# Kernel tuning notes

Measured on AMD Instinct MI355X. Metric: run time of the kernel, lower is better.

The kernel has to match this reference:

```python
import jax, jax.numpy as jnp
import numpy as np

HSP, WSP = 8, 32
HEADS = 6
EPS = 1e-5


def _ln(x, g, b):
    m = x.mean(-1, keepdims=True)
    v = ((x - m) ** 2).mean(-1, keepdims=True)
    return (x - m) / jnp.sqrt(v + EPS) * g + b


def _pos_mlp(rpe, pw0, pb0, g1, be1, w1, b1, g2, be2, w2, b2, g3, be3, w3, b3):
    # DynamicPosBias (residual=False): pos3(pos2(pos1(pos_proj(biases))))
    x = rpe @ pw0.T + pb0
    x = jax.nn.relu(_ln(x, g1, be1)) @ w1.T + b1
    x = jax.nn.relu(_ln(x, g2, be2)) @ w2.T + b2
    x = jax.nn.relu(_ln(x, g3, be3)) @ w3.T + b3
    return x  # (n_bias, HEADS)


def setup_inputs() -> dict:
    key = jax.random.key(0)
    ks = jax.random.split(key, 8)
    B, H, W, C = 4, 128, 256, 192
    L = H * W
    pd = (C // 4) // 4  # pos_dim = 12
    nbias = (2 * HSP - 1) * (2 * WSP - 1)  # 945
    N = HSP * WSP  # 256
    nW = L // N  # 128
    f32 = jnp.float32
    return {
        "qkv": jax.random.normal(ks[0], (3, B, L, C), f32),
        "mask": jax.random.normal(ks[1], (nW, N, N), f32),
        "rpe_biases": jax.random.normal(ks[2], (nbias, 2), f32),
        "pw0": jax.random.normal(ks[3], (pd, 2), f32) * 0.02,
        "pb0": jnp.zeros((pd,), f32),
        "g1": jnp.ones((pd,), f32),
        "be1": jnp.zeros((pd,), f32),
        "w1": jax.random.normal(ks[4], (pd, pd), f32) * 0.02,
        "b1": jnp.zeros((pd,), f32),
        "g2": jnp.ones((pd,), f32),
        "be2": jnp.zeros((pd,), f32),
        "w2": jax.random.normal(ks[5], (pd, pd), f32) * 0.02,
        "b2": jnp.zeros((pd,), f32),
        "g3": jnp.ones((pd,), f32),
        "be3": jnp.zeros((pd,), f32),
        "w3": jax.random.normal(ks[6], (HEADS, pd), f32) * 0.02,
        "b3": jnp.zeros((HEADS,), f32),
        "rpi": jax.random.randint(ks[7], (N, N), 0, nbias),
        "H": H,
        "W": W,
    }


def reference(qkv, mask, rpe_biases, pw0, pb0, g1, be1, w1, b1, g2, be2, w2, b2, g3, be3, w3, b3, rpi, H, W):
    _, B, L, C = qkv.shape
    hd = C // HEADS
    scale = hd ** -0.5
    N = HSP * WSP

    def im2win(x):  # (B,L,C) -> (B*nW, HEADS, N, hd)
        x = x.reshape(B, H // HSP, HSP, W // WSP, WSP, C)
        x = x.transpose(0, 1, 3, 2, 4, 5).reshape(-1, N, HEADS, hd)
        return x.transpose(0, 2, 1, 3)

    q = im2win(qkv[0]) * scale
    k = im2win(qkv[1])
    v = im2win(qkv[2])
    attn = jnp.einsum('whnd,whmd->whnm', q, k)  # (B*nW, HEADS, N, N)
    pos = _pos_mlp(rpe_biases, pw0, pb0, g1, be1, w1, b1, g2, be2, w2, b2, g3, be3, w3, b3)
    rpb = pos[rpi.reshape(-1)].reshape(N, N, HEADS).transpose(2, 0, 1)  # (HEADS,N,N)
    attn = attn + rpb[None]
    nW = mask.shape[0]
    attn = attn.reshape(B, nW, HEADS, N, N) + mask[None, :, None]
    attn = jax.nn.softmax(attn, axis=-1).reshape(-1, HEADS, N, N)
    x = (attn @ v).transpose(0, 2, 1, 3).reshape(-1, N, C)  # (B*nW, N, C)
    # windows2img
    x = x.reshape(B, H // HSP, W // WSP, HSP, WSP, C).transpose(0, 1, 3, 2, 4, 5).reshape(B, H, W, C)
    return x
```

## Files before the change

### kernel.cpp

```cpp
#include <hip/hip_runtime.h>

#define EPS 1e-5f
#define SCALE 0.17677669529663687f

typedef __attribute__((ext_vector_type(8))) short bf16x8;
typedef __attribute__((ext_vector_type(4))) float f32x4;

__device__ __forceinline__ unsigned short f2bf(float f) {
  unsigned u = __float_as_uint(f);
  return (unsigned short)((u + 0x7FFFu + ((u >> 16) & 1u)) >> 16);
}
__device__ __forceinline__ float bf2f(unsigned short h) {
  return __uint_as_float(((unsigned)h) << 16);
}
__device__ __forceinline__ float bflo(unsigned u) { return __uint_as_float(u << 16); }
__device__ __forceinline__ float bfhi(unsigned u) { return __uint_as_float(u & 0xFFFF0000u); }

__device__ __forceinline__ int bias_sidx(int row, int col) {
  return ((row >> 2) << 10) + ((col >> 5) << 7) + ((col & 15) << 3) + (((col >> 4) & 1) << 2) + (row & 3);
}

__global__ void pos_mlp_kernel(const float* __restrict__ rpe,
                               const float* __restrict__ pw0, const float* __restrict__ pb0,
                               const float* __restrict__ g1, const float* __restrict__ be1,
                               const float* __restrict__ w1, const float* __restrict__ b1,
                               const float* __restrict__ g2, const float* __restrict__ be2,
                               const float* __restrict__ w2, const float* __restrict__ b2,
                               const float* __restrict__ g3, const float* __restrict__ be3,
                               const float* __restrict__ w3, const float* __restrict__ b3,
                               float* __restrict__ posT) {
  int r = blockIdx.x * blockDim.x + threadIdx.x;
  if (r >= 945) return;
  float a = rpe[2 * r], c = rpe[2 * r + 1];
  float x[12], y[12];
#pragma unroll
  for (int i = 0; i < 12; ++i) x[i] = pw0[2 * i] * a + pw0[2 * i + 1] * c + pb0[i];

  auto stage = [&](const float* g, const float* be, const float* w, const float* bb,
                   const float* in, float* outv, int dout) {
    float m = 0.f;
#pragma unroll
    for (int i = 0; i < 12; ++i) m += in[i];
    m *= (1.f / 12.f);
    float v = 0.f;
#pragma unroll
    for (int i = 0; i < 12; ++i) { float d = in[i] - m; v += d * d; }
    v *= (1.f / 12.f);
    float rs = rsqrtf(v + EPS);
    float t[12];
#pragma unroll
    for (int i = 0; i < 12; ++i) t[i] = fmaxf((in[i] - m) * rs * g[i] + be[i], 0.f);
    for (int o = 0; o < dout; ++o) {
      float s = bb[o];
#pragma unroll
      for (int i = 0; i < 12; ++i) s += w[o * 12 + i] * t[i];
      outv[o] = s;
    }
  };
  stage(g1, be1, w1, b1, x, y, 12);
  stage(g2, be2, w2, b2, y, x, 12);
  stage(g3, be3, w3, b3, x, y, 6);
#pragma unroll
  for (int h = 0; h < 6; ++h) posT[h * 945 + r] = y[h];
}

__global__ void rpb_gather_swz(const int* __restrict__ rpi, const float* __restrict__ posT,
                               unsigned short* __restrict__ rpb) {
  int n2 = blockIdx.x * 256 + threadIdx.x;
  int row = n2 >> 8, col = n2 & 255;
  int idx = rpi[n2];
  int s = bias_sidx(row, col);
#pragma unroll
  for (int h = 0; h < 6; ++h) rpb[(h << 16) + s] = f2bf(posT[h * 945 + idx]);
}

__global__ void mask_cvt_swz(const float* __restrict__ src, uint4* __restrict__ dst) {
  int g = blockIdx.x * 256 + threadIdx.x;
  int wimg = g >> 13;
  int rem = g & 8191;
  int rg = rem >> 7;
  int cc = (rem >> 4) & 7;
  int l16 = rem & 15;
  const float* m = src + (wimg << 16);
  unsigned v[8];
#pragma unroll
  for (int ct = 0; ct < 2; ++ct)
#pragma unroll
    for (int r = 0; r < 4; ++r)
      v[ct * 4 + r] = f2bf(m[(rg * 4 + r) * 256 + cc * 32 + ct * 16 + l16]);
  uint4 o;
  o.x = v[0] | (v[1] << 16);
  o.y = v[2] | (v[3] << 16);
  o.z = v[4] | (v[5] << 16);
  o.w = v[6] | (v[7] << 16);
  dst[(wimg << 13) + (rg << 7) + (cc << 4) + l16] = o;
}

template <int USEBF>
__global__ __launch_bounds__(512, 4) void attn_kernel(
    const float* __restrict__ qkv, const float* __restrict__ maskf,
    const unsigned short* __restrict__ maskb, const unsigned short* __restrict__ rpb,
    float* __restrict__ out) {
  __shared__ unsigned short Kb[10240];
  __shared__ unsigned short Vt[8448];
  __shared__ unsigned short Pl[10240];

  const int tid = threadIdx.x;
  const int wv = tid >> 6;
  const int lane = tid & 63;
  const int quad = lane >> 4;
  const int l16 = lane & 15;
  const int wIdx = blockIdx.x, h = blockIdx.y;
  const int b = wIdx >> 7, wimg = wIdx & 127;
  const int wh = wimg >> 3, ww = wimg & 7;

  {
    const int tok = tid >> 3;
    const int c4 = (tid & 7) << 2;
#pragma unroll
    for (int p = 0; p < 4; ++p) {
      int n = (p << 6) + tok;
      int i = n >> 5, j = n & 31;
      int l = ((wh << 3) + i) * 256 + (ww << 5) + j;
      const float* kp = qkv + ((size_t)((4 + b) * 32768 + l)) * 192 + h * 32 + c4;
      const float* vp = qkv + ((size_t)((8 + b) * 32768 + l)) * 192 + h * 32 + c4;
      float4 kk = *(const float4*)kp;
      float4 vvv = *(const float4*)vp;
      unsigned long long pk = (unsigned long long)f2bf(kk.x) |
                              ((unsigned long long)f2bf(kk.y) << 16) |
                              ((unsigned long long)f2bf(kk.z) << 32) |
                              ((unsigned long long)f2bf(kk.w) << 48);
      *(unsigned long long*)(&Kb[n * 40 + c4]) = pk;
      int tokp = (n & ~31) | (((n & 15) << 1) + ((n >> 4) & 1));
      Vt[(c4 + 0) * 264 + tokp] = f2bf(vvv.x);
      Vt[(c4 + 1) * 264 + tokp] = f2bf(vvv.y);
      Vt[(c4 + 2) * 264 + tokp] = f2bf(vvv.z);
      Vt[(c4 + 3) * 264 + tokp] = f2bf(vvv.w);
    }
  }

  bf16x8 qf[2];
#pragma unroll
  for (int rt = 0; rt < 2; ++rt) {
    int n = (wv << 5) + (rt << 4) + l16;
    int i = n >> 5, j = n & 31;
    int l = ((wh << 3) + i) * 256 + (ww << 5) + j;
    const float* qp = qkv + ((size_t)(b * 32768 + l)) * 192 + h * 32 + (quad << 3);
    float4 a0 = *(const float4*)qp;
    float4 a1 = *(const float4*)(qp + 4);
    bf16x8 f;
    f[0] = (short)f2bf(a0.x * SCALE); f[1] = (short)f2bf(a0.y * SCALE);
    f[2] = (short)f2bf(a0.z * SCALE); f[3] = (short)f2bf(a0.w * SCALE);
    f[4] = (short)f2bf(a1.x * SCALE); f[5] = (short)f2bf(a1.y * SCALE);
    f[6] = (short)f2bf(a1.z * SCALE); f[7] = (short)f2bf(a1.w * SCALE);
    qf[rt] = f;
  }

  __syncthreads();

  f32x4 Oacc[2][2];
#pragma unroll
  for (int rt = 0; rt < 2; ++rt) {
    Oacc[rt][0] = (f32x4){0.f, 0.f, 0.f, 0.f};
    Oacc[rt][1] = (f32x4){0.f, 0.f, 0.f, 0.f};
  }
  float lsum[2][4] = {};

  const uint4* mb4 = (const uint4*)maskb + ((size_t)wimg << 13);
  const uint4* rb4 = (const uint4*)rpb + ((size_t)h << 13);
  const float* mfp0 = maskf + ((size_t)wimg << 16);
  unsigned short* Plw = &Pl[wv * 1280];
  const f32x4 zero = (f32x4){0.f, 0.f, 0.f, 0.f};

  for (int cc = 0; cc < 8; ++cc) {
    const int cb = cc << 5;
    uint4 mu[2], ru[2];
#pragma unroll
    for (int rt = 0; rt < 2; ++rt) {
      int rg = (wv << 3) + (rt << 2) + quad;
      int bidx = (rg << 7) + (cc << 4) + l16;
      ru[rt] = rb4[bidx];
      if (USEBF) mu[rt] = mb4[bidx];
    }
    bf16x8 kf0 = *(const bf16x8*)(&Kb[(cb + l16) * 40 + (quad << 3)]);
    bf16x8 kf1 = *(const bf16x8*)(&Kb[(cb + 16 + l16) * 40 + (quad << 3)]);
    f32x4 S[2][2];
#pragma unroll
    for (int rt = 0; rt < 2; ++rt) {
      S[rt][0] = __builtin_amdgcn_mfma_f32_16x16x32_bf16(qf[rt], kf0, zero, 0, 0, 0);
      S[rt][1] = __builtin_amdgcn_mfma_f32_16x16x32_bf16(qf[rt], kf1, zero, 0, 0, 0);
    }
#pragma unroll
    for (int rt = 0; rt < 2; ++rt) {
      float m0[4], m1[4], p0[4], p1[4];
      if (USEBF) {
        m0[0] = bflo(mu[rt].x); m0[1] = bfhi(mu[rt].x); m0[2] = bflo(mu[rt].y); m0[3] = bfhi(mu[rt].y);
        m1[0] = bflo(mu[rt].z); m1[1] = bfhi(mu[rt].z); m1[2] = bflo(mu[rt].w); m1[3] = bfhi(mu[rt].w);
      } else {
        int row0 = (wv << 5) + (rt << 4) + (quad << 2);
#pragma unroll
        for (int r = 0; r < 4; ++r) {
          m0[r] = mfp0[(row0 + r) * 256 + cb + l16];
          m1[r] = mfp0[(row0 + r) * 256 + cb + 16 + l16];
        }
      }
      p0[0] = bflo(ru[rt].x); p0[1] = bfhi(ru[rt].x); p0[2] = bflo(ru[rt].y); p0[3] = bfhi(ru[rt].y);
      p1[0] = bflo(ru[rt].z); p1[1] = bfhi(ru[rt].z); p1[2] = bflo(ru[rt].w); p1[3] = bfhi(ru[rt].w);
#pragma unroll
      for (int r = 0; r < 4; ++r) {
        float e0 = __expf(S[rt][0][r] + m0[r] + p0[r]);
        float e1 = __expf(S[rt][1][r] + m1[r] + p1[r]);
        lsum[rt][r] += e0 + e1;
        unsigned pw = (unsigned)f2bf(e0) | ((unsigned)f2bf(e1) << 16);
        *(unsigned*)(&Plw[((rt << 4) + (quad << 2) + r) * 40 + (l16 << 1)]) = pw;
      }
    }
    bf16x8 pf[2];
#pragma unroll
    for (int rt = 0; rt < 2; ++rt)
      pf[rt] = *(const bf16x8*)(&Plw[((rt << 4) + l16) * 40 + (quad << 3)]);
    bf16x8 vf0 = *(const bf16x8*)(&Vt[l16 * 264 + cb + (quad << 3)]);
    bf16x8 vf1 = *(const bf16x8*)(&Vt[(16 + l16) * 264 + cb + (quad << 3)]);
#pragma unroll
    for (int rt = 0; rt < 2; ++rt) {
      Oacc[rt][0] = __builtin_amdgcn_mfma_f32_16x16x32_bf16(pf[rt], vf0, Oacc[rt][0], 0, 0, 0);
      Oacc[rt][1] = __builtin_amdgcn_mfma_f32_16x16x32_bf16(pf[rt], vf1, Oacc[rt][1], 0, 0, 0);
    }
  }

#pragma unroll
  for (int rt = 0; rt < 2; ++rt) {
    int n0 = (wv << 5) + (rt << 4) + (quad << 2);
#pragma unroll
    for (int r = 0; r < 4; ++r) {
      float v = lsum[rt][r];
      v += __shfl_xor(v, 1);
      v += __shfl_xor(v, 2);
      v += __shfl_xor(v, 4);
      v += __shfl_xor(v, 8);
      float inv = 1.0f / v;
      int n = n0 + r;
      int i = n >> 5, j = n & 31;
      size_t o = ((size_t)((b * 128 + (wh << 3) + i) * 256 + (ww << 5) + j)) * 192 + h * 32 + l16;
      out[o] = Oacc[rt][0][r] * inv;
      out[o + 16] = Oacc[rt][1][r] * inv;
    }
  }
}

extern "C" void kernel_launch(void* const* d_in, const int* in_sizes, int n_in,
                              void* d_out, int out_size, void* d_ws, size_t ws_size,
                              hipStream_t stream) {
  const float* qkv = (const float*)d_in[0];
  const float* mask = (const float*)d_in[1];
  const float* rpe = (const float*)d_in[2];
  const float* pw0 = (const float*)d_in[3];
  const float* pb0 = (const float*)d_in[4];
  const float* g1 = (const float*)d_in[5];
  const float* be1 = (const float*)d_in[6];
  const float* w1 = (const float*)d_in[7];
  const float* b1 = (const float*)d_in[8];
  const float* g2 = (const float*)d_in[9];
  const float* be2 = (const float*)d_in[10];
  const float* w2 = (const float*)d_in[11];
  const float* b2 = (const float*)d_in[12];
  const float* g3 = (const float*)d_in[13];
  const float* be3 = (const float*)d_in[14];
  const float* w3 = (const float*)d_in[15];
  const float* b3 = (const float*)d_in[16];
  const int* rpi = (const int*)d_in[17];
  float* out = (float*)d_out;

  char* ws = (char*)d_ws;
  float* posT = (float*)ws;
  unsigned short* rpb = (unsigned short*)(ws + 22784);
  unsigned short* mb = (unsigned short*)(ws + 22784 + 786432);
  const size_t need_mb = 22784 + 786432 + 16777216;
  const int use_bf = (ws_size >= need_mb) ? 1 : 0;

  pos_mlp_kernel<<<4, 256, 0, stream>>>(rpe, pw0, pb0, g1, be1, w1, b1, g2, be2, w2, b2,
                                        g3, be3, w3, b3, posT);
  rpb_gather_swz<<<256, 256, 0, stream>>>(rpi, posT, rpb);
  if (use_bf)
    mask_cvt_swz<<<4096, 256, 0, stream>>>(mask, (uint4*)mb);

  dim3 grid(512, 6);
  if (use_bf)
    attn_kernel<1><<<grid, 512, 0, stream>>>(qkv, mask, mb, rpb, out);
  else
    attn_kernel<0><<<grid, 512, 0, stream>>>(qkv, mask, mb, rpb, out);
}
```

Baseline: 540.6 us.

## Compute S transposed to keep P in registers, use exp2 with log2e prefolding

Swaps the QK^T MFMA operands so the score tile comes out transposed, letting the exponentiated probabilities feed the PV MFMA straight from registers and dropping the per-wave LDS round-trip and its buffer. K rows are permuted in LDS and the mask and bias tables are re-swizzled to match the new fragment ownership. log2(e) is folded into the Q scale, the mask and the bias tables so exp2 can replace expf. Occupancy hint is raised to 6 and setprio is placed around the MFMAs. The row-sum reduction now needs a cross-lane shuffle to fetch each row's inverse, and the many coupled index changes must line up exactly.

```diff
diff --git a/kernel.cpp b/kernel.cpp
--- a/kernel.cpp
+++ b/kernel.cpp
@@ -1,24 +1,24 @@
 #include <hip/hip_runtime.h>
 
 #define EPS 1e-5f
-#define SCALE 0.17677669529663687f
+#define LOG2E 1.4426950408889634f
+#define QSCALE (0.17677669529663687f * 1.4426950408889634f)
 
 typedef __attribute__((ext_vector_type(8))) short bf16x8;
 typedef __attribute__((ext_vector_type(4))) float f32x4;
+
+#if __has_builtin(__builtin_amdgcn_exp2f)
+#define EXP2F(x) __builtin_amdgcn_exp2f(x)
+#else
+#define EXP2F(x) exp2f(x)
+#endif
 
 __device__ __forceinline__ unsigned short f2bf(float f) {
   unsigned u = __float_as_uint(f);
   return (unsigned short)((u + 0x7FFFu + ((u >> 16) & 1u)) >> 16);
 }
-__device__ __forceinline__ float bf2f(unsigned short h) {
-  return __uint_as_float(((unsigned)h) << 16);
-}
 __device__ __forceinline__ float bflo(unsigned u) { return __uint_as_float(u << 16); }
 __device__ __forceinline__ float bfhi(unsigned u) { return __uint_as_float(u & 0xFFFF0000u); }
-
-__device__ __forceinline__ int bias_sidx(int row, int col) {
-  return ((row >> 2) << 10) + ((col >> 5) << 7) + ((col & 15) << 3) + (((col >> 4) & 1) << 2) + (row & 3);
-}
 
 __global__ void pos_mlp_kernel(const float* __restrict__ rpe,
                                const float* __restrict__ pw0, const float* __restrict__ pb0,
@@ -67,43 +67,37 @@
 __global__ void rpb_gather_swz(const int* __restrict__ rpi, const float* __restrict__ posT,
                                unsigned short* __restrict__ rpb) {
   int n2 = blockIdx.x * 256 + threadIdx.x;
-  int row = n2 >> 8, col = n2 & 255;
+  int q = n2 >> 8, key = n2 & 255;
   int idx = rpi[n2];
-  int s = bias_sidx(row, col);
-#pragma unroll
-  for (int h = 0; h < 6; ++h) rpb[(h << 16) + s] = f2bf(posT[h * 945 + idx]);
+  int s = ((key >> 5) << 13) + (q << 5) + (key & 31);
+#pragma unroll
+  for (int h = 0; h < 6; ++h) rpb[(h << 16) + s] = f2bf(posT[h * 945 + idx] * LOG2E);
 }
 
 __global__ void mask_cvt_swz(const float* __restrict__ src, uint4* __restrict__ dst) {
   int g = blockIdx.x * 256 + threadIdx.x;
   int wimg = g >> 13;
   int rem = g & 8191;
-  int rg = rem >> 7;
-  int cc = (rem >> 4) & 7;
-  int l16 = rem & 15;
-  const float* m = src + (wimg << 16);
-  unsigned v[8];
-#pragma unroll
-  for (int ct = 0; ct < 2; ++ct)
-#pragma unroll
-    for (int r = 0; r < 4; ++r)
-      v[ct * 4 + r] = f2bf(m[(rg * 4 + r) * 256 + cc * 32 + ct * 16 + l16]);
-  uint4 o;
-  o.x = v[0] | (v[1] << 16);
-  o.y = v[2] | (v[3] << 16);
-  o.z = v[4] | (v[5] << 16);
-  o.w = v[6] | (v[7] << 16);
-  dst[(wimg << 13) + (rg << 7) + (cc << 4) + l16] = o;
+  int q = rem >> 5;
+  int k8 = rem & 31;
+  const float* m = src + ((size_t)wimg << 16) + (q << 8) + (k8 << 3);
+  float4 a0 = *(const float4*)m;
+  float4 a1 = *(const float4*)(m + 4);
+  unsigned v0 = (unsigned)f2bf(a0.x * LOG2E) | ((unsigned)f2bf(a0.y * LOG2E) << 16);
+  unsigned v1 = (unsigned)f2bf(a0.z * LOG2E) | ((unsigned)f2bf(a0.w * LOG2E) << 16);
+  unsigned v2 = (unsigned)f2bf(a1.x * LOG2E) | ((unsigned)f2bf(a1.y * LOG2E) << 16);
+  unsigned v3 = (unsigned)f2bf(a1.z * LOG2E) | ((unsigned)f2bf(a1.w * LOG2E) << 16);
+  uint4 o; o.x = v0; o.y = v1; o.z = v2; o.w = v3;
+  dst[(((size_t)wimg << 16) + ((k8 >> 2) << 13) + (q << 5) + ((k8 & 3) << 3)) >> 3] = o;
 }
 
 template <int USEBF>
-__global__ __launch_bounds__(512, 4) void attn_kernel(
+__global__ __launch_bounds__(512, 6) void attn_kernel(
     const float* __restrict__ qkv, const float* __restrict__ maskf,
     const unsigned short* __restrict__ maskb, const unsigned short* __restrict__ rpb,
     float* __restrict__ out) {
   __shared__ unsigned short Kb[10240];
   __shared__ unsigned short Vt[8448];
-  __shared__ unsigned short Pl[10240];
 
   const int tid = threadIdx.x;
   const int wv = tid >> 6;
@@ -130,12 +124,13 @@
                               ((unsigned long long)f2bf(kk.y) << 16) |
                               ((unsigned long long)f2bf(kk.z) << 32) |
                               ((unsigned long long)f2bf(kk.w) << 48);
-      *(unsigned long long*)(&Kb[n * 40 + c4]) = pk;
-      int tokp = (n & ~31) | (((n & 15) << 1) + ((n >> 4) & 1));
-      Vt[(c4 + 0) * 264 + tokp] = f2bf(vvv.x);
-      Vt[(c4 + 1) * 264 + tokp] = f2bf(vvv.y);
-      Vt[(c4 + 2) * 264 + tokp] = f2bf(vvv.z);
-      Vt[(c4 + 3) * 264 + tokp] = f2bf(vvv.w);
+      int c = n & 31;
+      int rowp = (n & ~31) | ((c & 4) << 2) | ((c & 24) >> 1) | (c & 3);
+      *(unsigned long long*)(&Kb[rowp * 40 + c4]) = pk;
+      Vt[(c4 + 0) * 264 + n] = f2bf(vvv.x);
+      Vt[(c4 + 1) * 264 + n] = f2bf(vvv.y);
+      Vt[(c4 + 2) * 264 + n] = f2bf(vvv.z);
+      Vt[(c4 + 3) * 264 + n] = f2bf(vvv.w);
     }
   }
 
@@ -149,10 +144,10 @@
     float4 a0 = *(const float4*)qp;
     float4 a1 = *(const float4*)(qp + 4);
     bf16x8 f;
-    f[0] = (short)f2bf(a0.x * SCALE); f[1] = (short)f2bf(a0.y * SCALE);
-    f[2] = (short)f2bf(a0.z * SCALE); f[3] = (short)f2bf(a0.w * SCALE);
-    f[4] = (short)f2bf(a1.x * SCALE); f[5] = (short)f2bf(a1.y * SCALE);
-    f[6] = (short)f2bf(a1.z * SCALE); f[7] = (short)f2bf(a1.w * SCALE);
+    f[0] = (short)f2bf(a0.x * QSCALE); f[1] = (short)f2bf(a0.y * QSCALE);
+    f[2] = (short)f2bf(a0.z * QSCALE); f[3] = (short)f2bf(a0.w * QSCALE);
+    f[4] = (short)f2bf(a1.x * QSCALE); f[5] = (short)f2bf(a1.y * QSCALE);
+    f[6] = (short)f2bf(a1.z * QSCALE); f[7] = (short)f2bf(a1.w * QSCALE);
     qf[rt] = f;
   }
 
@@ -164,86 +159,85 @@
     Oacc[rt][0] = (f32x4){0.f, 0.f, 0.f, 0.f};
     Oacc[rt][1] = (f32x4){0.f, 0.f, 0.f, 0.f};
   }
-  float lsum[2][4] = {};
-
-  const uint4* mb4 = (const uint4*)maskb + ((size_t)wimg << 13);
-  const uint4* rb4 = (const uint4*)rpb + ((size_t)h << 13);
+  float lsum[2] = {0.f, 0.f};
+
+  const unsigned short* rp = rpb + ((size_t)h << 16);
+  const unsigned short* mp = maskb + ((size_t)wimg << 16);
   const float* mfp0 = maskf + ((size_t)wimg << 16);
-  unsigned short* Plw = &Pl[wv * 1280];
+  const int boff = (((wv << 5) + l16) << 5) + (quad << 3);
   const f32x4 zero = (f32x4){0.f, 0.f, 0.f, 0.f};
 
   for (int cc = 0; cc < 8; ++cc) {
     const int cb = cc << 5;
-    uint4 mu[2], ru[2];
+    const int tof = cc << 13;
+    uint4 pr[2], mr[2];
 #pragma unroll
     for (int rt = 0; rt < 2; ++rt) {
-      int rg = (wv << 3) + (rt << 2) + quad;
-      int bidx = (rg << 7) + (cc << 4) + l16;
-      ru[rt] = rb4[bidx];
-      if (USEBF) mu[rt] = mb4[bidx];
+      int o0 = tof + boff + (rt << 9);
+      pr[rt] = *(const uint4*)(rp + o0);
+      if (USEBF) mr[rt] = *(const uint4*)(mp + o0);
     }
     bf16x8 kf0 = *(const bf16x8*)(&Kb[(cb + l16) * 40 + (quad << 3)]);
     bf16x8 kf1 = *(const bf16x8*)(&Kb[(cb + 16 + l16) * 40 + (quad << 3)]);
-    f32x4 S[2][2];
-#pragma unroll
-    for (int rt = 0; rt < 2; ++rt) {
-      S[rt][0] = __builtin_amdgcn_mfma_f32_16x16x32_bf16(qf[rt], kf0, zero, 0, 0, 0);
-      S[rt][1] = __builtin_amdgcn_mfma_f32_16x16x32_bf16(qf[rt], kf1, zero, 0, 0, 0);
-    }
-#pragma unroll
-    for (int rt = 0; rt < 2; ++rt) {
-      float m0[4], m1[4], p0[4], p1[4];
-      if (USEBF) {
-        m0[0] = bflo(mu[rt].x); m0[1] = bfhi(mu[rt].x); m0[2] = bflo(mu[rt].y); m0[3] = bfhi(mu[rt].y);
-        m1[0] = bflo(mu[rt].z); m1[1] = bfhi(mu[rt].z); m1[2] = bflo(mu[rt].w); m1[3] = bfhi(mu[rt].w);
-      } else {
-        int row0 = (wv << 5) + (rt << 4) + (quad << 2);
-#pragma unroll
-        for (int r = 0; r < 4; ++r) {
-          m0[r] = mfp0[(row0 + r) * 256 + cb + l16];
-          m1[r] = mfp0[(row0 + r) * 256 + cb + 16 + l16];
-        }
-      }
-      p0[0] = bflo(ru[rt].x); p0[1] = bfhi(ru[rt].x); p0[2] = bflo(ru[rt].y); p0[3] = bfhi(ru[rt].y);
-      p1[0] = bflo(ru[rt].z); p1[1] = bfhi(ru[rt].z); p1[2] = bflo(ru[rt].w); p1[3] = bfhi(ru[rt].w);
-#pragma unroll
-      for (int r = 0; r < 4; ++r) {
-        float e0 = __expf(S[rt][0][r] + m0[r] + p0[r]);
-        float e1 = __expf(S[rt][1][r] + m1[r] + p1[r]);
-        lsum[rt][r] += e0 + e1;
-        unsigned pw = (unsigned)f2bf(e0) | ((unsigned)f2bf(e1) << 16);
-        *(unsigned*)(&Plw[((rt << 4) + (quad << 2) + r) * 40 + (l16 << 1)]) = pw;
-      }
-    }
-    bf16x8 pf[2];
-#pragma unroll
-    for (int rt = 0; rt < 2; ++rt)
-      pf[rt] = *(const bf16x8*)(&Plw[((rt << 4) + l16) * 40 + (quad << 3)]);
     bf16x8 vf0 = *(const bf16x8*)(&Vt[l16 * 264 + cb + (quad << 3)]);
     bf16x8 vf1 = *(const bf16x8*)(&Vt[(16 + l16) * 264 + cb + (quad << 3)]);
 #pragma unroll
     for (int rt = 0; rt < 2; ++rt) {
-      Oacc[rt][0] = __builtin_amdgcn_mfma_f32_16x16x32_bf16(pf[rt], vf0, Oacc[rt][0], 0, 0, 0);
-      Oacc[rt][1] = __builtin_amdgcn_mfma_f32_16x16x32_bf16(pf[rt], vf1, Oacc[rt][1], 0, 0, 0);
+      __builtin_amdgcn_s_setprio(1);
+      f32x4 S0 = __builtin_amdgcn_mfma_f32_16x16x32_bf16(kf0, qf[rt], zero, 0, 0, 0);
+      f32x4 S1 = __builtin_amdgcn_mfma_f32_16x16x32_bf16(kf1, qf[rt], zero, 0, 0, 0);
+      __builtin_amdgcn_s_setprio(0);
+      float m_[8], p_[8];
+      if (USEBF) {
+        m_[0] = bflo(mr[rt].x); m_[1] = bfhi(mr[rt].x);
+        m_[2] = bflo(mr[rt].y); m_[3] = bfhi(mr[rt].y);
+        m_[4] = bflo(mr[rt].z); m_[5] = bfhi(mr[rt].z);
+        m_[6] = bflo(mr[rt].w); m_[7] = bfhi(mr[rt].w);
+      } else {
+        int qrow = (wv << 5) + (rt << 4) + l16;
+        float4 f0 = *(const float4*)(mfp0 + (qrow << 8) + cb + (quad << 3));
+        float4 f1 = *(const float4*)(mfp0 + (qrow << 8) + cb + (quad << 3) + 4);
+        m_[0] = f0.x * LOG2E; m_[1] = f0.y * LOG2E; m_[2] = f0.z * LOG2E; m_[3] = f0.w * LOG2E;
+        m_[4] = f1.x * LOG2E; m_[5] = f1.y * LOG2E; m_[6] = f1.z * LOG2E; m_[7] = f1.w * LOG2E;
+      }
+      p_[0] = bflo(pr[rt].x); p_[1] = bfhi(pr[rt].x);
+      p_[2] = bflo(pr[rt].y); p_[3] = bfhi(pr[rt].y);
+      p_[4] = bflo(pr[rt].z); p_[5] = bfhi(pr[rt].z);
+      p_[6] = bflo(pr[rt].w); p_[7] = bfhi(pr[rt].w);
+      float e[8];
+#pragma unroll
+      for (int r = 0; r < 4; ++r) {
+        e[r]     = EXP2F(S0[r] + m_[r] + p_[r]);
+        e[4 + r] = EXP2F(S1[r] + m_[4 + r] + p_[4 + r]);
+      }
+      lsum[rt] += ((e[0] + e[1]) + (e[2] + e[3])) + ((e[4] + e[5]) + (e[6] + e[7]));
+      union PF { unsigned w[4]; bf16x8 v; } u;
+      u.w[0] = (unsigned)f2bf(e[0]) | ((unsigned)f2bf(e[1]) << 16);
+      u.w[1] = (unsigned)f2bf(e[2]) | ((unsigned)f2bf(e[3]) << 16);
+      u.w[2] = (unsigned)f2bf(e[4]) | ((unsigned)f2bf(e[5]) << 16);
+      u.w[3] = (unsigned)f2bf(e[6]) | ((unsigned)f2bf(e[7]) << 16);
+      __builtin_amdgcn_s_setprio(1);
+      Oacc[rt][0] = __builtin_amdgcn_mfma_f32_16x16x32_bf16(u.v, vf0, Oacc[rt][0], 0, 0, 0);
+      Oacc[rt][1] = __builtin_amdgcn_mfma_f32_16x16x32_bf16(u.v, vf1, Oacc[rt][1], 0, 0, 0);
+      __builtin_amdgcn_s_setprio(0);
     }
   }
 
 #pragma unroll
   for (int rt = 0; rt < 2; ++rt) {
+    float v = lsum[rt];
+    v += __shfl_xor(v, 16);
+    v += __shfl_xor(v, 32);
+    float inv = 1.0f / v;
     int n0 = (wv << 5) + (rt << 4) + (quad << 2);
 #pragma unroll
     for (int r = 0; r < 4; ++r) {
-      float v = lsum[rt][r];
-      v += __shfl_xor(v, 1);
-      v += __shfl_xor(v, 2);
-      v += __shfl_xor(v, 4);
-      v += __shfl_xor(v, 8);
-      float inv = 1.0f / v;
+      float ir = __shfl(inv, (quad << 4) + (quad << 2) + r);
       int n = n0 + r;
       int i = n >> 5, j = n & 31;
       size_t o = ((size_t)((b * 128 + (wh << 3) + i) * 256 + (ww << 5) + j)) * 192 + h * 32 + l16;
-      out[o] = Oacc[rt][0][r] * inv;
-      out[o + 16] = Oacc[rt][1][r] * inv;
+      out[o] = Oacc[rt][0][r] * ir;
+      out[o + 16] = Oacc[rt][1][r] * ir;
     }
   }
 }
```

Measured after the change: 568.4 us. +5.2%, slower.
